# Kernel optimization log

Hardware: AMD Instinct MI355X
Metric: run time of the kernel (lower is better)

## Reference

```python
import jax, jax.numpy as jnp
import numpy as np

B, T, I, U, S = 1024, 256, 64, 1024, 64  # batch, warmup_len, num_input_signals, units, output_steps


def setup_inputs() -> dict:
    key = jax.random.key(0)
    ks = jax.random.split(key, 4)
    s = lambda n: 1.0 / np.sqrt(n)
    inputs = jax.random.normal(ks[0], (B, T, I), jnp.float32)
    Wk = jax.random.normal(ks[1], (I, 4 * U), jnp.float32) * s(I)   # input kernel (gate order i,f,g,o)
    Wr = jax.random.normal(ks[2], (U, 4 * U), jnp.float32) * s(U)   # recurrent kernel
    b = jnp.zeros((4 * U,), jnp.float32)
    Wd = jax.random.normal(ks[3], (U, I), jnp.float32) * s(U)       # dense head
    bd = jnp.zeros((I,), jnp.float32)
    output_indices = jnp.arange(2, dtype=jnp.int32)
    return {"inputs": inputs, "Wk": Wk, "Wr": Wr, "b": b, "Wd": Wd, "bd": bd,
            "output_indices": output_indices, "output_steps": S}


def _lstm_step(h, c, x, Wk, Wr, b):
    # Keras LSTMCell math, gate order i, f, g(candidate), o
    z = x @ Wk + h @ Wr + b
    i, f, g, o = jnp.split(z, 4, axis=-1)
    c = jax.nn.sigmoid(f) * c + jax.nn.sigmoid(i) * jnp.tanh(g)
    h = jax.nn.sigmoid(o) * jnp.tanh(c)
    return h, c


def reference(inputs, Wk, Wr, b, Wd, bd, output_indices, output_steps):
    Bn = inputs.shape[0]
    Un = Wr.shape[0]
    h0 = jnp.zeros((Bn, Un), inputs.dtype)
    c0 = jnp.zeros((Bn, Un), inputs.dtype)

    # warmup: run LSTM over the input sequence, keep final state only
    def warm(carry, x_t):
        h, c = carry
        h, c = _lstm_step(h, c, x_t, Wk, Wr, b)
        return (h, c), None

    (h, c), _ = jax.lax.scan(warm, (h0, c0), jnp.swapaxes(inputs, 0, 1))
    pred = h @ Wd + bd  # first prediction [B, I]

    def dec(carry, _):
        h, c, p = carry
        h, c = _lstm_step(h, c, p, Wk, Wr, b)
        p = h @ Wd + bd
        return (h, c, p), p

    _, rest = jax.lax.scan(dec, (h, c, pred), None, length=output_steps - 1)
    preds = jnp.concatenate([pred[None], rest], axis=0)   # [S, B, I]
    preds = jnp.swapaxes(preds, 0, 1)                     # [B, S, I]
    return jnp.take(preds, output_indices, axis=-1)       # [B, S, len(output_indices)]
```

## Files before the change

kernel.cpp:

```cpp
#include <hip/hip_runtime.h>
#include <hip/hip_bf16.h>
#include <stdint.h>


typedef _Float16 f16;
typedef _Float16 f16x8 __attribute__((ext_vector_type(8)));
typedef float f32x4 __attribute__((ext_vector_type(4)));

#define TILE_HALVES 8192
#define NKZ 17
#define NKD 16

__device__ __forceinline__ int swz(int r, int k) { return (r * 64 + k) ^ ((r & 7) << 3); }

__device__ __forceinline__ void stage8k(const f16* __restrict__ g, f16* l, int tid) {
  const int wave = tid >> 6, lane = tid & 63;
  const char* gp = (const char*)g;
  char* lp = (char*)l;
#pragma unroll
  for (int i = 0; i < 4; i++) {
    const int off = i * 4096 + wave * 1024;
    __builtin_amdgcn_global_load_lds(
        (const __attribute__((address_space(1))) unsigned int*)(gp + off + lane * 16),
        (__attribute__((address_space(3))) unsigned int*)(lp + off), 16, 0, 0);
  }
}
__device__ __forceinline__ void stage4k(const f16* __restrict__ g, f16* l, int tid) {
  const int wave = tid >> 6, lane = tid & 63;
  const char* gp = (const char*)g;
  char* lp = (char*)l;
#pragma unroll
  for (int i = 0; i < 2; i++) {
    const int off = i * 4096 + wave * 1024;
    __builtin_amdgcn_global_load_lds(
        (const __attribute__((address_space(1))) unsigned int*)(gp + off + lane * 16),
        (__attribute__((address_space(3))) unsigned int*)(lp + off), 16, 0, 0);
  }
}

__device__ __forceinline__ float sigf(float x) { return 1.0f / (1.0f + __expf(-x)); }
__device__ __forceinline__ float tanhfast(float x) { return 1.0f - 2.0f / (__expf(2.0f * x) + 1.0f); }

__global__ void __launch_bounds__(256, 2) lstm_step(
    const f16* __restrict__ Wp, const f16* __restrict__ Ax,
    const f16* __restrict__ hin, f16* __restrict__ hout,
    float* __restrict__ c32p, const float* __restrict__ bperm,
    const float* __restrict__ Wd, const int* __restrict__ oidx,
    float* __restrict__ outp, int n_idx, int nkz) {
  const int tid = threadIdx.x;
  const int bid = blockIdx.x;
  const int xcd = bid & 7;
  const int ni = 4 * xcd + ((bid >> 3) & 3);
  const int mi = bid >> 5;

  __shared__ __align__(16) f16 As[3][4096];
  __shared__ __align__(16) f16 Bs[3][8192];

  const int has_x = (Ax != nullptr) ? 1 : 0;
  const f16* Ax0 = Ax + (size_t)(mi >> 1) * TILE_HALVES + (mi & 1) * 4096;
  const f16* Ah0 = hin + (size_t)(mi >> 1) * 16 * TILE_HALVES + (mi & 1) * 4096;
  const f16* Wb = Wp + (size_t)ni * nkz * TILE_HALVES;

  f32x4 acc[2][4];
#pragma unroll
  for (int a = 0; a < 2; a++)
#pragma unroll
    for (int q = 0; q < 4; q++) acc[a][q] = (f32x4){0.f, 0.f, 0.f, 0.f};

  auto atile = [&](int kk) -> const f16* {
    return (kk == 0 && has_x) ? Ax0 : (Ah0 + (size_t)(kk - has_x) * TILE_HALVES);
  };

  stage4k(atile(0), As[0], tid);
  stage8k(Wb, Bs[0], tid);
  stage4k(atile(1), As[1], tid);
  stage8k(Wb + TILE_HALVES, Bs[1], tid);

  const int w = tid >> 6, lane = tid & 63;
  const int rw = w >> 1, cw = w & 1, ln15 = lane & 15, ln4 = lane >> 4;

  int cur = 0;
  for (int kk = 0; kk < nkz; kk++) {
    if (kk + 1 < nkz) {
      asm volatile("s_waitcnt vmcnt(6)" ::: "memory");
    } else {
      asm volatile("s_waitcnt vmcnt(0)" ::: "memory");
    }
    __builtin_amdgcn_s_barrier();
    if (kk + 2 < nkz) {
      int wr = cur + 2; if (wr >= 3) wr -= 3;
      stage4k(atile(kk + 2), As[wr], tid);
      stage8k(Wb + (size_t)(kk + 2) * TILE_HALVES, Bs[wr], tid);
    }
    const f16* Ab = As[cur];
    const f16* Bb = Bs[cur];
#pragma unroll
    for (int kc = 0; kc < 2; kc++) {
      const int kb = kc * 32 + ln4 * 8;
      f16x8 af[2], bf[4];
#pragma unroll
      for (int mf = 0; mf < 2; mf++) {
        const int r = 32 * rw + 16 * mf + ln15;
        af[mf] = *(const f16x8*)(Ab + swz(r, kb));
      }
#pragma unroll
      for (int nf = 0; nf < 4; nf++) {
        const int n = 64 * cw + 16 * nf + ln15;
        bf[nf] = *(const f16x8*)(Bb + swz(n, kb));
      }
      __builtin_amdgcn_s_setprio(1);
#pragma unroll
      for (int mf = 0; mf < 2; mf++)
#pragma unroll
        for (int nf = 0; nf < 4; nf++)
          acc[mf][nf] = __builtin_amdgcn_mfma_f32_16x16x32_f16(af[mf], bf[nf], acc[mf][nf], 0, 0, 0);
      __builtin_amdgcn_s_setprio(0);
    }
    cur = cur + 1; if (cur == 3) cur = 0;
  }

  const int u_glob = 32 * ni + 16 * cw + ln15;
  const int kkh = u_glob >> 6, kh = u_glob & 63;
  f16* ob = hout + ((size_t)(mi >> 1) * 16 + kkh) * TILE_HALVES;
  const float bi0 = bperm[ni * 128 + 64 * cw + 0 + ln15];
  const float bi1 = bperm[ni * 128 + 64 * cw + 16 + ln15];
  const float bi2 = bperm[ni * 128 + 64 * cw + 32 + ln15];
  const float bi3 = bperm[ni * 128 + 64 * cw + 48 + ln15];

  float* cp = c32p + ((size_t)bid * 256 + tid) * 8;
  f32x4 cold0 = *(const f32x4*)(cp);
  f32x4 cold1 = *(const f32x4*)(cp + 4);

  float hv[2][4];
#pragma unroll
  for (int mf = 0; mf < 2; mf++) {
    f32x4 cn4;
#pragma unroll
    for (int reg = 0; reg < 4; reg++) {
      const int rl = 32 * rw + 16 * mf + 4 * ln4 + reg;
      const int r128 = (mi & 1) * 64 + rl;
      const float zi = acc[mf][0][reg] + bi0;
      const float zf = acc[mf][1][reg] + bi1;
      const float zg = acc[mf][2][reg] + bi2;
      const float zo = acc[mf][3][reg] + bi3;
      const float co = (mf == 0) ? cold0[reg] : cold1[reg];
      const float cn = sigf(zf) * co + sigf(zi) * tanhfast(zg);
      const float hn = sigf(zo) * tanhfast(cn);
      cn4[reg] = cn;
      hv[mf][reg] = hn;
      ob[swz(r128, kh)] = (f16)hn;
    }
    *(f32x4*)(cp + mf * 4) = cn4;
  }

  if (outp != nullptr) {
    const int ostride = 64 * n_idx;
    for (int j = 0; j < n_idx; j++) {
      const float wdj = Wd[(size_t)u_glob * 64 + oidx[j]];
#pragma unroll
      for (int mf = 0; mf < 2; mf++)
#pragma unroll
        for (int reg = 0; reg < 4; reg++) {
          float v = hv[mf][reg] * wdj;
          v += __shfl_xor(v, 1);
          v += __shfl_xor(v, 2);
          v += __shfl_xor(v, 4);
          v += __shfl_xor(v, 8);
          if (ln15 == 0) {
            const int brow = 64 * mi + 32 * rw + 16 * mf + 4 * ln4 + reg;
            atomicAdd(&outp[(size_t)brow * ostride + j], v);
          }
        }
    }
  }
}

__global__ void __launch_bounds__(256) prep_W(const float* __restrict__ Wk,
                                              const float* __restrict__ Wr,
                                              f16* __restrict__ W16) {
  const int blk = blockIdx.x;
  const int ni = blk / NKZ, kk = blk % NKZ;
  f16* ob = W16 + (size_t)blk * TILE_HALVES;
  for (int c = threadIdx.x; c < 1024; c += 256) {
    const int n = c >> 3, k0 = (c & 7) * 8;
    const int nf = n >> 4, j = n & 15;
    const int gate = nf & 3;
    const int u = 32 * ni + 16 * (nf >> 2) + j;
    const int col = gate * 1024 + u;
    f16x8 v;
#pragma unroll
    for (int e = 0; e < 8; e++) {
      const int kr = kk * 64 + k0 + e;
      const float val = (kr < 64) ? Wk[(size_t)kr * 4096 + col]
                                  : Wr[(size_t)(kr - 64) * 4096 + col];
      v[e] = (f16)val;
    }
    *(f16x8*)(ob + swz(n, k0)) = v;
  }
}

__global__ void __launch_bounds__(256) prep_Wp(const float* __restrict__ Wk,
                                               const float* __restrict__ Wr,
                                               const float* __restrict__ Wd,
                                               f16* __restrict__ WP16) {
  const int blk = blockIdx.x;
  const int ni = blk / NKD, kk = blk % NKD;
  f16* ob = WP16 + (size_t)blk * TILE_HALVES;
  for (int c = threadIdx.x; c < 1024; c += 256) {
    const int n = c >> 3, k0 = (c & 7) * 8;
    const int nf = n >> 4, j = n & 15;
    const int gate = nf & 3;
    const int u = 32 * ni + 16 * (nf >> 2) + j;
    const int col = gate * 1024 + u;
    const int uh0 = kk * 64 + k0;
    float accv[8];
#pragma unroll
    for (int e = 0; e < 8; e++) accv[e] = Wr[(size_t)(uh0 + e) * 4096 + col];
#pragma unroll
    for (int i = 0; i < 64; i++) {
      const float wki = Wk[(size_t)i * 4096 + col];
#pragma unroll
      for (int e = 0; e < 8; e++)
        accv[e] += Wd[(size_t)(uh0 + e) * 64 + i] * wki;
    }
    f16x8 v;
#pragma unroll
    for (int e = 0; e < 8; e++) v[e] = (f16)accv[e];
    *(f16x8*)(ob + swz(n, k0)) = v;
  }
}

__global__ void __launch_bounds__(256) prep_X(const float* __restrict__ inp, f16* __restrict__ X16) {
  const int blk = blockIdx.x;
  const int t = blk >> 3, mi = blk & 7;
  f16* ob = X16 + (size_t)blk * TILE_HALVES;
  for (int c = threadIdx.x; c < 1024; c += 256) {
    const int r = c >> 3, k0 = (c & 7) * 8;
    const int b = 128 * mi + r;
    const float* src = inp + (size_t)b * 16384 + t * 64 + k0;
    const float4 x0 = *(const float4*)(src);
    const float4 x1 = *(const float4*)(src + 4);
    f16x8 v;
    v[0] = (f16)x0.x; v[1] = (f16)x0.y; v[2] = (f16)x0.z; v[3] = (f16)x0.w;
    v[4] = (f16)x1.x; v[5] = (f16)x1.y; v[6] = (f16)x1.z; v[7] = (f16)x1.w;
    *(f16x8*)(ob + swz(r, k0)) = v;
  }
}

__global__ void __launch_bounds__(256) prep_b(const float* __restrict__ b, float* __restrict__ bperm) {
  const int x = blockIdx.x * 256 + threadIdx.x;
  const int ni = x >> 7, rem = x & 127, nf = rem >> 4, j = rem & 15;
  bperm[x] = b[(nf & 3) * 1024 + 32 * ni + 16 * (nf >> 2) + j];
}

__global__ void __launch_bounds__(256) prep_b2(const float* __restrict__ b,
                                               const float* __restrict__ bd,
                                               const float* __restrict__ Wk,
                                               float* __restrict__ bperm2) {
  const int x = blockIdx.x * 256 + threadIdx.x;
  const int ni = x >> 7, rem = x & 127, nf = rem >> 4, j = rem & 15;
  const int col = (nf & 3) * 1024 + 32 * ni + 16 * (nf >> 2) + j;
  float acc = b[col];
#pragma unroll
  for (int i = 0; i < 64; i++) acc += bd[i] * Wk[(size_t)i * 4096 + col];
  bperm2[x] = acc;
}

__global__ void __launch_bounds__(256) out_init(float* __restrict__ out,
                                                const float* __restrict__ bd,
                                                const int* __restrict__ oidx,
                                                int n_idx, int total) {
  const int x = blockIdx.x * 256 + threadIdx.x;
  if (x < total) out[x] = bd[oidx[x % n_idx]];
}

extern "C" void kernel_launch(void* const* d_in, const int* in_sizes, int n_in,
                              void* d_out, int out_size, void* d_ws, size_t ws_size,
                              hipStream_t stream) {
  const float* inputs = (const float*)d_in[0];
  const float* Wk = (const float*)d_in[1];
  const float* Wr = (const float*)d_in[2];
  const float* bv = (const float*)d_in[3];
  const float* Wd = (const float*)d_in[4];
  const float* bd = (const float*)d_in[5];
  const int* oidx = (const int*)d_in[6];
  float* out = (float*)d_out;
  const int n_idx = out_size / (1024 * 64);
  if (n_idx < 1) return;

  char* ws = (char*)d_ws;
  const size_t OFF_W16 = 0;
  const size_t OFF_BPERM = 8912896;
  const size_t OFF_C32 = 8929280;
  const size_t OFF_H0 = 13123584;
  const size_t OFF_H1 = 15220736;
  const size_t OFF_X16 = 17317888;
  const size_t NEED = 50872320;
  if (ws_size < NEED) return;

  f16* W16 = (f16*)(ws + OFF_W16);
  float* bperm = (float*)(ws + OFF_BPERM);
  float* c32p = (float*)(ws + OFF_C32);
  f16* hb[2] = {(f16*)(ws + OFF_H0), (f16*)(ws + OFF_H1)};
  f16* X16 = (f16*)(ws + OFF_X16);
  f16* WP16 = (f16*)(ws + OFF_X16);
  float* bperm2 = (float*)(ws + OFF_X16 + 8388608);

  hipMemsetAsync(hb[0], 0, 2097152, stream);
  hipMemsetAsync(c32p, 0, 4194304, stream);
  hipLaunchKernelGGL(prep_W, dim3(544), dim3(256), 0, stream, Wk, Wr, W16);
  hipLaunchKernelGGL(prep_b, dim3(16), dim3(256), 0, stream, bv, bperm);
  hipLaunchKernelGGL(prep_X, dim3(2048), dim3(256), 0, stream, inputs, X16);
  {
    const int total = 1024 * 64 * n_idx;
    hipLaunchKernelGGL(out_init, dim3((total + 255) / 256), dim3(256), 0, stream,
                       out, bd, oidx, n_idx, total);
  }

  for (int t = 0; t < 319; ++t) {
    if (t == 256) {
      hipLaunchKernelGGL(prep_Wp, dim3(512), dim3(256), 0, stream, Wk, Wr, Wd, WP16);
      hipLaunchKernelGGL(prep_b2, dim3(16), dim3(256), 0, stream, bv, bd, Wk, bperm2);
    }
    const bool warm = (t < 256);
    const f16* W = warm ? W16 : WP16;
    const f16* Axp = warm ? (X16 + (size_t)t * 8 * TILE_HALVES) : nullptr;
    const float* bp = warm ? bperm : bperm2;
    float* op = (t >= 255) ? (out + (size_t)(t - 255) * n_idx) : nullptr;
    hipLaunchKernelGGL(lstm_step, dim3(512), dim3(256), 0, stream,
                       W, Axp, (const f16*)hb[t & 1], hb[(t + 1) & 1],
                       c32p, bp, Wd, oidx, op, n_idx, warm ? NKZ : NKD);
  }
}
```

Measured before the change: 6.235 ms.

## Replace per-timestep launches with a persistent LSTM kernel and per-XCD barriers

Replaces the 319 separate step launches with one persistent kernel of 256 blocks. Blocks are grouped per XCD through an atomic rank counter, and each XCD owns a 128-row batch slice synchronized by a spin barrier on global atomics. The cell state stays in registers across steps, and input conversion is done on the fly by one block per XCD. Output projections now go through partial-sum buffers that are reduced on the next step instead of atomics. This is meant to remove launch overhead and the global c-state traffic. The risks are that correctness depends on every block being co-resident and on the hardware XCC id being evenly distributed, on top of the spin-wait cost.

```diff
diff --git a/kernel.cpp b/kernel.cpp
--- a/kernel.cpp
+++ b/kernel.cpp
@@ -7,171 +7,251 @@
 typedef _Float16 f16x8 __attribute__((ext_vector_type(8)));
 typedef float f32x4 __attribute__((ext_vector_type(4)));
 
+#define NKW 17
+#define NKD 16
 #define TILE_HALVES 8192
-#define NKZ 17
-#define NKD 16
 
 __device__ __forceinline__ int swz(int r, int k) { return (r * 64 + k) ^ ((r & 7) << 3); }
 
-__device__ __forceinline__ void stage8k(const f16* __restrict__ g, f16* l, int tid) {
-  const int wave = tid >> 6, lane = tid & 63;
-  const char* gp = (const char*)g;
-  char* lp = (char*)l;
+template <int AUX>
+__device__ __forceinline__ void stage_q(const f16* __restrict__ g, f16* l, int w, int lane) {
+  const char* gp = (const char*)g + w * 4096 + lane * 16;
+  char* lp = (char*)l + w * 4096;
 #pragma unroll
   for (int i = 0; i < 4; i++) {
-    const int off = i * 4096 + wave * 1024;
     __builtin_amdgcn_global_load_lds(
-        (const __attribute__((address_space(1))) unsigned int*)(gp + off + lane * 16),
-        (__attribute__((address_space(3))) unsigned int*)(lp + off), 16, 0, 0);
-  }
-}
-__device__ __forceinline__ void stage4k(const f16* __restrict__ g, f16* l, int tid) {
-  const int wave = tid >> 6, lane = tid & 63;
-  const char* gp = (const char*)g;
-  char* lp = (char*)l;
-#pragma unroll
-  for (int i = 0; i < 2; i++) {
-    const int off = i * 4096 + wave * 1024;
-    __builtin_amdgcn_global_load_lds(
-        (const __attribute__((address_space(1))) unsigned int*)(gp + off + lane * 16),
-        (__attribute__((address_space(3))) unsigned int*)(lp + off), 16, 0, 0);
+        (const __attribute__((address_space(1))) unsigned int*)(gp + i * 1024),
+        (__attribute__((address_space(3))) unsigned int*)(lp + i * 1024), 16, 0, AUX);
   }
 }
 
 __device__ __forceinline__ float sigf(float x) { return 1.0f / (1.0f + __expf(-x)); }
 __device__ __forceinline__ float tanhfast(float x) { return 1.0f - 2.0f / (__expf(2.0f * x) + 1.0f); }
 
-__global__ void __launch_bounds__(256, 2) lstm_step(
-    const f16* __restrict__ Wp, const f16* __restrict__ Ax,
-    const f16* __restrict__ hin, f16* __restrict__ hout,
-    float* __restrict__ c32p, const float* __restrict__ bperm,
-    const float* __restrict__ Wd, const int* __restrict__ oidx,
-    float* __restrict__ outp, int n_idx, int nkz) {
+__global__ void __launch_bounds__(256, 1) lstm_persist(
+    const f16* __restrict__ W16, const f16* __restrict__ WP16,
+    const float* __restrict__ inputs,
+    f16* __restrict__ hb0, f16* __restrict__ hb1, f16* __restrict__ xbuf,
+    float* __restrict__ ppart,
+    const float* __restrict__ bperm, const float* __restrict__ bperm2,
+    const float* __restrict__ Wd, const float* __restrict__ bd,
+    const int* __restrict__ oidx, float* __restrict__ out,
+    int n_idx, unsigned* __restrict__ bar) {
   const int tid = threadIdx.x;
-  const int bid = blockIdx.x;
-  const int xcd = bid & 7;
-  const int ni = 4 * xcd + ((bid >> 3) & 3);
-  const int mi = bid >> 5;
-
-  __shared__ __align__(16) f16 As[3][4096];
-  __shared__ __align__(16) f16 Bs[3][8192];
-
-  const int has_x = (Ax != nullptr) ? 1 : 0;
-  const f16* Ax0 = Ax + (size_t)(mi >> 1) * TILE_HALVES + (mi & 1) * 4096;
-  const f16* Ah0 = hin + (size_t)(mi >> 1) * 16 * TILE_HALVES + (mi & 1) * 4096;
-  const f16* Wb = Wp + (size_t)ni * nkz * TILE_HALVES;
-
-  f32x4 acc[2][4];
-#pragma unroll
-  for (int a = 0; a < 2; a++)
-#pragma unroll
-    for (int q = 0; q < 4; q++) acc[a][q] = (f32x4){0.f, 0.f, 0.f, 0.f};
-
-  auto atile = [&](int kk) -> const f16* {
-    return (kk == 0 && has_x) ? Ax0 : (Ah0 + (size_t)(kk - has_x) * TILE_HALVES);
-  };
-
-  stage4k(atile(0), As[0], tid);
-  stage8k(Wb, Bs[0], tid);
-  stage4k(atile(1), As[1], tid);
-  stage8k(Wb + TILE_HALVES, Bs[1], tid);
+
+  __shared__ __align__(16) f16 As[3][TILE_HALVES];
+  __shared__ __align__(16) f16 Bs[3][TILE_HALVES];
+  __shared__ unsigned rank_sh;
+
+  unsigned xcd;
+  asm("s_getreg_b32 %0, hwreg(HW_REG_XCC_ID)" : "=s"(xcd));
+  xcd &= 7u;
+  unsigned* rank_ctr = bar;
+  unsigned* bar_cnt = bar + 128;
+  unsigned* bar_gen = bar + 256;
+  if (tid == 0)
+    rank_sh = __hip_atomic_fetch_add(&rank_ctr[xcd * 16], 1u, __ATOMIC_RELAXED,
+                                     __HIP_MEMORY_SCOPE_AGENT) & 31u;
+  __syncthreads();
+  const int mi = (int)xcd;
+  const int ni = (int)rank_sh;
 
   const int w = tid >> 6, lane = tid & 63;
   const int rw = w >> 1, cw = w & 1, ln15 = lane & 15, ln4 = lane >> 4;
-
-  int cur = 0;
-  for (int kk = 0; kk < nkz; kk++) {
-    if (kk + 1 < nkz) {
-      asm volatile("s_waitcnt vmcnt(6)" ::: "memory");
-    } else {
-      asm volatile("s_waitcnt vmcnt(0)" ::: "memory");
-    }
-    __builtin_amdgcn_s_barrier();
-    if (kk + 2 < nkz) {
-      int wr = cur + 2; if (wr >= 3) wr -= 3;
-      stage4k(atile(kk + 2), As[wr], tid);
-      stage8k(Wb + (size_t)(kk + 2) * TILE_HALVES, Bs[wr], tid);
-    }
-    const f16* Ab = As[cur];
-    const f16* Bb = Bs[cur];
-#pragma unroll
-    for (int kc = 0; kc < 2; kc++) {
-      const int kb = kc * 32 + ln4 * 8;
-      f16x8 af[2], bf[4];
-#pragma unroll
-      for (int mf = 0; mf < 2; mf++) {
-        const int r = 32 * rw + 16 * mf + ln15;
-        af[mf] = *(const f16x8*)(Ab + swz(r, kb));
-      }
-#pragma unroll
-      for (int nf = 0; nf < 4; nf++) {
-        const int n = 64 * cw + 16 * nf + ln15;
-        bf[nf] = *(const f16x8*)(Bb + swz(n, kb));
-      }
-      __builtin_amdgcn_s_setprio(1);
-#pragma unroll
-      for (int mf = 0; mf < 2; mf++)
-#pragma unroll
-        for (int nf = 0; nf < 4; nf++)
-          acc[mf][nf] = __builtin_amdgcn_mfma_f32_16x16x32_f16(af[mf], bf[nf], acc[mf][nf], 0, 0, 0);
-      __builtin_amdgcn_s_setprio(0);
-    }
-    cur = cur + 1; if (cur == 3) cur = 0;
-  }
-
   const int u_glob = 32 * ni + 16 * cw + ln15;
   const int kkh = u_glob >> 6, kh = u_glob & 63;
-  f16* ob = hout + ((size_t)(mi >> 1) * 16 + kkh) * TILE_HALVES;
-  const float bi0 = bperm[ni * 128 + 64 * cw + 0 + ln15];
-  const float bi1 = bperm[ni * 128 + 64 * cw + 16 + ln15];
-  const float bi2 = bperm[ni * 128 + 64 * cw + 32 + ln15];
-  const float bi3 = bperm[ni * 128 + 64 * cw + 48 + ln15];
-
-  float* cp = c32p + ((size_t)bid * 256 + tid) * 8;
-  f32x4 cold0 = *(const f32x4*)(cp);
-  f32x4 cold1 = *(const f32x4*)(cp + 4);
-
-  float hv[2][4];
-#pragma unroll
-  for (int mf = 0; mf < 2; mf++) {
-    f32x4 cn4;
-#pragma unroll
-    for (int reg = 0; reg < 4; reg++) {
-      const int rl = 32 * rw + 16 * mf + 4 * ln4 + reg;
-      const int r128 = (mi & 1) * 64 + rl;
-      const float zi = acc[mf][0][reg] + bi0;
-      const float zf = acc[mf][1][reg] + bi1;
-      const float zg = acc[mf][2][reg] + bi2;
-      const float zo = acc[mf][3][reg] + bi3;
-      const float co = (mf == 0) ? cold0[reg] : cold1[reg];
-      const float cn = sigf(zf) * co + sigf(zi) * tanhfast(zg);
-      const float hn = sigf(zo) * tanhfast(cn);
-      cn4[reg] = cn;
-      hv[mf][reg] = hn;
-      ob[swz(r128, kh)] = (f16)hn;
-    }
-    *(f32x4*)(cp + mf * 4) = cn4;
-  }
-
-  if (outp != nullptr) {
-    const int ostride = 64 * n_idx;
-    for (int j = 0; j < n_idx; j++) {
-      const float wdj = Wd[(size_t)u_glob * 64 + oidx[j]];
-#pragma unroll
-      for (int mf = 0; mf < 2; mf++)
-#pragma unroll
-        for (int reg = 0; reg < 4; reg++) {
-          float v = hv[mf][reg] * wdj;
-          v += __shfl_xor(v, 1);
-          v += __shfl_xor(v, 2);
-          v += __shfl_xor(v, 4);
-          v += __shfl_xor(v, 8);
-          if (ln15 == 0) {
-            const int brow = 64 * mi + 32 * rw + 16 * mf + 4 * ln4 + reg;
-            atomicAdd(&outp[(size_t)brow * ostride + j], v);
+
+  float biw[4], bi2[4];
+#pragma unroll
+  for (int nf = 0; nf < 4; nf++) {
+    biw[nf] = bperm[ni * 128 + 64 * cw + 16 * nf + ln15];
+    bi2[nf] = bperm2[ni * 128 + 64 * cw + 16 * nf + ln15];
+  }
+  float wdj[8];
+#pragma unroll
+  for (int j = 0; j < 8; j++) wdj[j] = 0.f;
+  for (int j = 0; j < n_idx; j++) wdj[j] = Wd[(size_t)u_glob * 64 + oidx[j]];
+
+  float cst[4][4];
+#pragma unroll
+  for (int a = 0; a < 4; a++)
+#pragma unroll
+    for (int q = 0; q < 4; q++) cst[a][q] = 0.f;
+
+  for (int t = 0; t < 319; ++t) {
+    if (tid == 0 && t > 0) {
+      int guard = 0;
+      while (__hip_atomic_load(&bar_gen[xcd * 16], __ATOMIC_RELAXED,
+                               __HIP_MEMORY_SCOPE_AGENT) < (unsigned)t) {
+        __builtin_amdgcn_s_sleep(2);
+        if (++guard > (1 << 26)) break;
+      }
+    }
+    __builtin_amdgcn_s_barrier();
+
+    const bool warm = (t < 256);
+    const int nk = warm ? NKW : NKD;
+    const f16* Wb = warm ? (W16 + (size_t)ni * NKW * TILE_HALVES)
+                         : (WP16 + (size_t)ni * NKD * TILE_HALVES);
+    const f16* hin = (t & 1) ? hb1 : hb0;
+    f16* hout = (t & 1) ? hb0 : hb1;
+    const f16* hbase = hin + (size_t)mi * 16 * TILE_HALVES - (warm ? TILE_HALVES : 0);
+    const f16* xb = xbuf + (size_t)((t & 1) * 8 + mi) * TILE_HALVES;
+
+    if (t >= 256) {
+      const int s = t - 256;
+      const int sb = (t - 1) & 1;
+      if (tid < 4 * n_idx) {
+        const int row = 4 * ni + (tid & 3);
+        const int j = tid >> 2;
+        float acc = bd[oidx[j]];
+        for (int q = 0; q < 32; q++) {
+#pragma unroll
+          for (int c2 = 0; c2 < 2; c2++) {
+            const size_t idx = ((((size_t)(sb * 8 + mi) * 32 + q) * 8 + j) * 2 + c2) * 128 + row;
+            acc += __hip_atomic_load(&ppart[idx], __ATOMIC_RELAXED, __HIP_MEMORY_SCOPE_AGENT);
           }
         }
-    }
+        out[((size_t)(128 * mi + row) * 64 + s) * n_idx + j] = acc;
+      }
+      asm volatile("s_waitcnt vmcnt(0)" ::: "memory");
+    }
+
+    stage_q<1>((warm ? xb : hbase), As[0], w, lane);
+    stage_q<0>(Wb, Bs[0], w, lane);
+    stage_q<1>(hbase + TILE_HALVES, As[1], w, lane);
+    stage_q<0>(Wb + TILE_HALVES, Bs[1], w, lane);
+
+    f32x4 acc[4][4];
+#pragma unroll
+    for (int a = 0; a < 4; a++)
+#pragma unroll
+      for (int q = 0; q < 4; q++) acc[a][q] = (f32x4){0.f, 0.f, 0.f, 0.f};
+
+    for (int kk = 0; kk < nk; ++kk) {
+      if (kk == nk - 1) asm volatile("s_waitcnt vmcnt(0)" ::: "memory");
+      else              asm volatile("s_waitcnt vmcnt(8)" ::: "memory");
+      __builtin_amdgcn_s_barrier();
+      if (kk + 2 < nk) {
+        const int b2 = (kk + 2) % 3;
+        stage_q<1>(((kk + 2 == 0) ? xb : hbase + (size_t)(kk + 2) * TILE_HALVES), As[b2], w, lane);
+        stage_q<0>(Wb + (size_t)(kk + 2) * TILE_HALVES, Bs[b2], w, lane);
+      }
+      const f16* Ab = As[kk % 3];
+      const f16* Bb = Bs[kk % 3];
+#pragma unroll
+      for (int kc = 0; kc < 2; kc++) {
+        const int kb = kc * 32 + ln4 * 8;
+        f16x8 af[4], bf[4];
+#pragma unroll
+        for (int mf = 0; mf < 4; mf++)
+          af[mf] = *(const f16x8*)(Ab + swz(64 * rw + 16 * mf + ln15, kb));
+#pragma unroll
+        for (int nf = 0; nf < 4; nf++)
+          bf[nf] = *(const f16x8*)(Bb + swz(64 * cw + 16 * nf + ln15, kb));
+        __builtin_amdgcn_s_setprio(1);
+#pragma unroll
+        for (int mf = 0; mf < 4; mf++)
+#pragma unroll
+          for (int nf = 0; nf < 4; nf++)
+            acc[mf][nf] = __builtin_amdgcn_mfma_f32_16x16x32_f16(af[mf], bf[nf], acc[mf][nf], 0, 0, 0);
+        __builtin_amdgcn_s_setprio(0);
+      }
+    }
+
+    const float b0 = warm ? biw[0] : bi2[0];
+    const float b1 = warm ? biw[1] : bi2[1];
+    const float b2v = warm ? biw[2] : bi2[2];
+    const float b3 = warm ? biw[3] : bi2[3];
+    f16* ob = hout + ((size_t)mi * 16 + kkh) * TILE_HALVES;
+    float hv[4][4];
+#pragma unroll
+    for (int mf = 0; mf < 4; mf++) {
+#pragma unroll
+      for (int reg = 0; reg < 4; reg++) {
+        const int rl = 64 * rw + 16 * mf + 4 * ln4 + reg;
+        const float zi = acc[mf][0][reg] + b0;
+        const float zf = acc[mf][1][reg] + b1;
+        const float zg = acc[mf][2][reg] + b2v;
+        const float zo = acc[mf][3][reg] + b3;
+        const float cn = sigf(zf) * cst[mf][reg] + sigf(zi) * tanhfast(zg);
+        const float hn = sigf(zo) * tanhfast(cn);
+        cst[mf][reg] = cn;
+        hv[mf][reg] = hn;
+        ob[swz(rl, kh)] = (f16)hn;
+      }
+    }
+
+    if (t >= 255) {
+      const int sbw = t & 1;
+      for (int j = 0; j < n_idx; j++) {
+        const float wd = wdj[j];
+#pragma unroll
+        for (int mf = 0; mf < 4; mf++)
+#pragma unroll
+          for (int reg = 0; reg < 4; reg++) {
+            float v = hv[mf][reg] * wd;
+            v += __shfl_xor(v, 1);
+            v += __shfl_xor(v, 2);
+            v += __shfl_xor(v, 4);
+            v += __shfl_xor(v, 8);
+            if (ln15 == 0) {
+              const int rl = 64 * rw + 16 * mf + 4 * ln4 + reg;
+              const size_t idx = ((((size_t)(sbw * 8 + mi) * 32 + ni) * 8 + j) * 2 + cw) * 128 + rl;
+              ppart[idx] = v;
+            }
+          }
+      }
+    }
+
+    if (warm && (t + 1 < 256) && ni == 0) {
+      const int r = tid >> 1, k0 = (tid & 1) * 32;
+      const float* src = inputs + (size_t)(128 * mi + r) * 16384 + (size_t)(t + 1) * 64 + k0;
+      f16* xo = xbuf + (size_t)(((t + 1) & 1) * 8 + mi) * TILE_HALVES;
+#pragma unroll
+      for (int q = 0; q < 4; q++) {
+        const float4 a = *(const float4*)(src + q * 8);
+        const float4 bq = *(const float4*)(src + q * 8 + 4);
+        f16x8 v;
+        v[0] = (f16)a.x; v[1] = (f16)a.y; v[2] = (f16)a.z; v[3] = (f16)a.w;
+        v[4] = (f16)bq.x; v[5] = (f16)bq.y; v[6] = (f16)bq.z; v[7] = (f16)bq.w;
+        *(f16x8*)(xo + swz(r, k0 + 8 * q)) = v;
+      }
+    }
+
+    asm volatile("s_waitcnt vmcnt(0)" ::: "memory");
+    __builtin_amdgcn_s_barrier();
+    if (tid == 0) {
+      unsigned old = __hip_atomic_fetch_add(&bar_cnt[xcd * 16], 1u, __ATOMIC_RELAXED,
+                                            __HIP_MEMORY_SCOPE_AGENT);
+      if ((old & 31u) == 31u)
+        __hip_atomic_fetch_add(&bar_gen[xcd * 16], 1u, __ATOMIC_RELAXED,
+                               __HIP_MEMORY_SCOPE_AGENT);
+    }
+  }
+
+  if (tid == 0) {
+    int guard = 0;
+    while (__hip_atomic_load(&bar_gen[xcd * 16], __ATOMIC_RELAXED,
+                             __HIP_MEMORY_SCOPE_AGENT) < 319u) {
+      __builtin_amdgcn_s_sleep(2);
+      if (++guard > (1 << 26)) break;
+    }
+  }
+  __builtin_amdgcn_s_barrier();
+  if (tid < 4 * n_idx) {
+    const int row = 4 * ni + (tid & 3);
+    const int j = tid >> 2;
+    const int sb = 318 & 1;
+    float acc = bd[oidx[j]];
+    for (int q = 0; q < 32; q++) {
+#pragma unroll
+      for (int c2 = 0; c2 < 2; c2++) {
+        const size_t idx = ((((size_t)(sb * 8 + mi) * 32 + q) * 8 + j) * 2 + c2) * 128 + row;
+        acc += __hip_atomic_load(&ppart[idx], __ATOMIC_RELAXED, __HIP_MEMORY_SCOPE_AGENT);
+      }
+    }
+    out[((size_t)(128 * mi + row) * 64 + 63) * n_idx + j] = acc;
   }
 }
 
@@ -179,7 +259,7 @@
                                               const float* __restrict__ Wr,
                                               f16* __restrict__ W16) {
   const int blk = blockIdx.x;
-  const int ni = blk / NKZ, kk = blk % NKZ;
+  const int ni = blk / NKW, kk = blk % NKW;
   f16* ob = W16 + (size_t)blk * TILE_HALVES;
   for (int c = threadIdx.x; c < 1024; c += 256) {
     const int n = c >> 3, k0 = (c & 7) * 8;
@@ -230,23 +310,6 @@
   }
 }
 
-__global__ void __launch_bounds__(256) prep_X(const float* __restrict__ inp, f16* __restrict__ X16) {
-  const int blk = blockIdx.x;
-  const int t = blk >> 3, mi = blk & 7;
-  f16* ob = X16 + (size_t)blk * TILE_HALVES;
-  for (int c = threadIdx.x; c < 1024; c += 256) {
-    const int r = c >> 3, k0 = (c & 7) * 8;
-    const int b = 128 * mi + r;
-    const float* src = inp + (size_t)b * 16384 + t * 64 + k0;
-    const float4 x0 = *(const float4*)(src);
-    const float4 x1 = *(const float4*)(src + 4);
-    f16x8 v;
-    v[0] = (f16)x0.x; v[1] = (f16)x0.y; v[2] = (f16)x0.z; v[3] = (f16)x0.w;
-    v[4] = (f16)x1.x; v[5] = (f16)x1.y; v[6] = (f16)x1.z; v[7] = (f16)x1.w;
-    *(f16x8*)(ob + swz(r, k0)) = v;
-  }
-}
-
 __global__ void __launch_bounds__(256) prep_b(const float* __restrict__ b, float* __restrict__ bperm) {
   const int x = blockIdx.x * 256 + threadIdx.x;
   const int ni = x >> 7, rem = x & 127, nf = rem >> 4, j = rem & 15;
@@ -266,12 +329,20 @@
   bperm2[x] = acc;
 }
 
-__global__ void __launch_bounds__(256) out_init(float* __restrict__ out,
-                                                const float* __restrict__ bd,
-                                                const int* __restrict__ oidx,
-                                                int n_idx, int total) {
-  const int x = blockIdx.x * 256 + threadIdx.x;
-  if (x < total) out[x] = bd[oidx[x % n_idx]];
+__global__ void __launch_bounds__(256) prep_x0(const float* __restrict__ inp, f16* __restrict__ xbuf) {
+  const int mi = blockIdx.x, tid = threadIdx.x;
+  const int r = tid >> 1, k0 = (tid & 1) * 32;
+  const float* src = inp + (size_t)(128 * mi + r) * 16384 + k0;
+  f16* ob = xbuf + (size_t)mi * TILE_HALVES;
+#pragma unroll
+  for (int q = 0; q < 4; q++) {
+    const float4 a = *(const float4*)(src + q * 8);
+    const float4 b = *(const float4*)(src + q * 8 + 4);
+    f16x8 v;
+    v[0] = (f16)a.x; v[1] = (f16)a.y; v[2] = (f16)a.z; v[3] = (f16)a.w;
+    v[4] = (f16)b.x; v[5] = (f16)b.y; v[6] = (f16)b.z; v[7] = (f16)b.w;
+    *(f16x8*)(ob + swz(r, k0 + 8 * q)) = v;
+  }
 }
 
 extern "C" void kernel_launch(void* const* d_in, const int* in_sizes, int n_in,
@@ -286,49 +357,42 @@
   const int* oidx = (const int*)d_in[6];
   float* out = (float*)d_out;
   const int n_idx = out_size / (1024 * 64);
-  if (n_idx < 1) return;
+  if (n_idx < 1 || n_idx > 8) return;
 
   char* ws = (char*)d_ws;
   const size_t OFF_W16 = 0;
-  const size_t OFF_BPERM = 8912896;
-  const size_t OFF_C32 = 8929280;
-  const size_t OFF_H0 = 13123584;
-  const size_t OFF_H1 = 15220736;
-  const size_t OFF_X16 = 17317888;
-  const size_t NEED = 50872320;
+  const size_t OFF_WP = 8912896;
+  const size_t OFF_BPERM = 17301504;
+  const size_t OFF_BPERM2 = 17317888;
+  const size_t OFF_H0 = 17334272;
+  const size_t OFF_H1 = 19431424;
+  const size_t OFF_XB = 21528576;
+  const size_t OFF_PP = 21790720;
+  const size_t OFF_BAR = 25985024;
+  const size_t NEED = 25989120;
   if (ws_size < NEED) return;
 
   f16* W16 = (f16*)(ws + OFF_W16);
+  f16* WP16 = (f16*)(ws + OFF_WP);
   float* bperm = (float*)(ws + OFF_BPERM);
-  float* c32p = (float*)(ws + OFF_C32);
-  f16* hb[2] = {(f16*)(ws + OFF_H0), (f16*)(ws + OFF_H1)};
-  f16* X16 = (f16*)(ws + OFF_X16);
-  f16* WP16 = (f16*)(ws + OFF_X16);
-  float* bperm2 = (float*)(ws + OFF_X16 + 8388608);
-
-  hipMemsetAsync(hb[0], 0, 2097152, stream);
-  hipMemsetAsync(c32p, 0, 4194304, stream);
+  float* bperm2 = (float*)(ws + OFF_BPERM2);
+  f16* hb0 = (f16*)(ws + OFF_H0);
+  f16* hb1 = (f16*)(ws + OFF_H1);
+  f16* xbuf = (f16*)(ws + OFF_XB);
+  float* ppart = (float*)(ws + OFF_PP);
+  unsigned* bar = (unsigned*)(ws + OFF_BAR);
+
+  hipMemsetAsync(hb0, 0, 2097152, stream);
+  hipMemsetAsync(bar, 0, 4096, stream);
   hipLaunchKernelGGL(prep_W, dim3(544), dim3(256), 0, stream, Wk, Wr, W16);
+  hipLaunchKernelGGL(prep_Wp, dim3(512), dim3(256), 0, stream, Wk, Wr, Wd, WP16);
   hipLaunchKernelGGL(prep_b, dim3(16), dim3(256), 0, stream, bv, bperm);
-  hipLaunchKernelGGL(prep_X, dim3(2048), dim3(256), 0, stream, inputs, X16);
-  {
-    const int total = 1024 * 64 * n_idx;
-    hipLaunchKernelGGL(out_init, dim3((total + 255) / 256), dim3(256), 0, stream,
-                       out, bd, oidx, n_idx, total);
-  }
-
-  for (int t = 0; t < 319; ++t) {
-    if (t == 256) {
-      hipLaunchKernelGGL(prep_Wp, dim3(512), dim3(256), 0, stream, Wk, Wr, Wd, WP16);
-      hipLaunchKernelGGL(prep_b2, dim3(16), dim3(256), 0, stream, bv, bd, Wk, bperm2);
-    }
-    const bool warm = (t < 256);
-    const f16* W = warm ? W16 : WP16;
-    const f16* Axp = warm ? (X16 + (size_t)t * 8 * TILE_HALVES) : nullptr;
-    const float* bp = warm ? bperm : bperm2;
-    float* op = (t >= 255) ? (out + (size_t)(t - 255) * n_idx) : nullptr;
-    hipLaunchKernelGGL(lstm_step, dim3(512), dim3(256), 0, stream,
-                       W, Axp, (const f16*)hb[t & 1], hb[(t + 1) & 1],
-                       c32p, bp, Wd, oidx, op, n_idx, warm ? NKZ : NKD);
-  }
-}
+  hipLaunchKernelGGL(prep_b2, dim3(16), dim3(256), 0, stream, bv, bd, Wk, bperm2);
+  hipLaunchKernelGGL(prep_x0, dim3(8), dim3(256), 0, stream, inputs, xbuf);
+
+  hipLaunchKernelGGL(lstm_persist, dim3(256), dim3(256), 0, stream,
+                     (const f16*)W16, (const f16*)WP16, inputs,
+                     hb0, hb1, xbuf, ppart,
+                     (const float*)bperm, (const float*)bperm2,
+                     Wd, bd, oidx, out, n_idx, bar);
+}
```

Result: slower. 8.204 ms (+31.6%).
